# Optimization experiments

Hardware: AMD Instinct MI355X
Metric: run time of the kernel (lower is better)

## Reference

```python
import jax, jax.numpy as jnp
import numpy as np

BATCH = 32      # init batch_size
HID = 256       # init hidden_dim
SENT = 64       # sentence_size
WORDS = 64      # words per sentence (the -1 in the view)
N = BATCH * SENT


def setup_inputs() -> dict:
    key = jax.random.key(0)
    k1, k2, k3, k4 = jax.random.split(key, 4)
    stdv_lin = 1.0 / np.sqrt(HID)
    x = jax.random.normal(k1, (N, WORDS, HID), dtype=jnp.float32)
    W = jax.random.uniform(k2, (HID, HID), jnp.float32, -stdv_lin, stdv_lin)
    b = jax.random.uniform(k3, (HID,), jnp.float32, -stdv_lin, stdv_lin)
    context = jax.random.uniform(k4, (HID,), jnp.float32, -stdv_lin, stdv_lin)
    return {"x": x, "W": W, "b": b, "context": context, "sentence_size": SENT}


def reference(x, W, b, context, sentence_size):
    # tanh(Linear(x)) applied per position; vectorized over the batch loop
    attends = jnp.tanh(jnp.einsum("nwh,oh->nwo", x, W) + b)  # [N, WORDS, HID]
    scores = attends * context                                 # [N, WORDS, HID]
    # nn.Softmax on the [-1, HID] view -> softmax over the hidden dim
    alpha = jax.nn.softmax(scores, axis=-1)                    # [N, WORDS, HID]
    attended = x * alpha                                       # legacy same-numel mul
    attended = attended.reshape(BATCH, sentence_size, -1, HID)
    return jnp.sum(attended, axis=2)                           # [BATCH, SENT, HID]
```

## Files before the change

kernel.cpp:

```cpp
#include <hip/hip_runtime.h>
#include <hip/hip_bf16.h>

#define HID 256
#define NROWS 2048
#define NITER 8
#define GRID (NROWS / NITER)
#define PITCH 264
#define AS1 __attribute__((address_space(1)))
#define AS3 __attribute__((address_space(3)))

typedef __attribute__((ext_vector_type(8))) short short8;
typedef __attribute__((ext_vector_type(4))) float float4v;
typedef __attribute__((ext_vector_type(4))) unsigned short ushort4v;

__device__ __forceinline__ float bf2f(unsigned short u) {
    return __uint_as_float(((unsigned int)u) << 16);
}

__device__ __forceinline__ unsigned int pk_bf16(float a, float b) {
    __hip_bfloat162 p = __float22bfloat162_rn(float2{a, b});
    return *(unsigned int*)&p;
}

__device__ __forceinline__ float tanh_fast(float x) {
    float e = __builtin_amdgcn_exp2f(x * 2.8853900817779268f);
    return 1.0f - 2.0f * __builtin_amdgcn_rcpf(e + 1.0f);
}

__device__ __forceinline__ float exp_small(float s) {
    float p = __builtin_fmaf(s, 0.16666667f, 0.5f);
    p = __builtin_fmaf(p, s, 1.0f);
    return __builtin_fmaf(p, s, 1.0f);
}

__device__ __forceinline__ float row16_sum(float v) {
    float t;
    t = __builtin_bit_cast(float, __builtin_amdgcn_update_dpp(
            0, __builtin_bit_cast(int, v), 0xB1, 0xf, 0xf, true));
    v += t;
    t = __builtin_bit_cast(float, __builtin_amdgcn_update_dpp(
            0, __builtin_bit_cast(int, v), 0x4E, 0xf, 0xf, true));
    v += t;
    t = __builtin_bit_cast(float, __builtin_amdgcn_update_dpp(
            0, __builtin_bit_cast(int, v), 0x124, 0xf, 0xf, true));
    v += t;
    t = __builtin_bit_cast(float, __builtin_amdgcn_update_dpp(
            0, __builtin_bit_cast(int, v), 0x128, 0xf, 0xf, true));
    v += t;
    return v;
}

__global__ void cvt_w(const float* __restrict__ W, unsigned short* __restrict__ Wb) {
    int i = blockIdx.x * 256 + threadIdx.x;
    float4v v = ((const float4v*)W)[i];
    unsigned int lo = pk_bf16(v.x, v.y), hi = pk_bf16(v.z, v.w);
    ushort4v u;
    u.x = (unsigned short)lo; u.y = (unsigned short)(lo >> 16);
    u.z = (unsigned short)hi; u.w = (unsigned short)(hi >> 16);
    ((ushort4v*)Wb)[i] = u;
}

__global__ __launch_bounds__(512, 2) void attend_fused(
    const float* __restrict__ x, const unsigned short* __restrict__ Wb,
    const float* __restrict__ bias, const float* __restrict__ ctx,
    float* __restrict__ out)
{
    __shared__ float fstage[64 * 256];
    __shared__ unsigned short xs[64 * PITCH];
    __shared__ float wsum[8][64];
    __shared__ float rinv[64];

    const int tid  = threadIdx.x;
    const int wave = tid >> 6;
    const int lane = tid & 63;
    const int q    = lane >> 4;
    const int c    = lane & 15;
    const int obase = wave * 32;

    float bb[2], cc[2];
#pragma unroll
    for (int nt = 0; nt < 2; ++nt) {
        bb[nt] = bias[obase + 2 * c + nt];
        cc[nt] = ctx[obase + 2 * c + nt];
    }
    short8 bfrag[8][2];
#pragma unroll
    for (int nt = 0; nt < 2; ++nt) {
        const unsigned short* wr = &Wb[(size_t)(obase + 2 * c + nt) * 256 + q * 8];
#pragma unroll
        for (int kt = 0; kt < 8; ++kt)
            bfrag[kt][nt] = *(const short8*)(wr + kt * 32);
    }

    const int n0 = blockIdx.x * NITER;

    {
        const float* xn = x + (size_t)n0 * (64 * 256);
#pragma unroll
        for (int t = 0; t < 8; ++t) {
            const int row = wave * 8 + t;
            __builtin_amdgcn_global_load_lds((const AS1 void*)(xn + row * 256 + lane * 4),
                                             (AS3 void*)&fstage[row * 256], 16, 0, 0);
        }
    }

    for (int it = 0; it < NITER; ++it) {
        const int n = n0 + it;
        const float* xnext = x + (size_t)(n + 1) * (64 * 256);
        const bool pf = (it + 1 < NITER);

        __syncthreads();

#pragma unroll
        for (int i = 0; i < 8; ++i) {
            const int chunk = tid + 512 * i;
            const int r = chunk >> 6, col4 = (chunk & 63) * 4;
            float4v v = *(const float4v*)&fstage[chunk * 4];
            uint2 u;
            u.x = pk_bf16(v.x, v.y);
            u.y = pk_bf16(v.z, v.w);
            *(uint2*)&xs[r * PITCH + col4] = u;
        }
        __syncthreads();

        if (pf) {
#pragma unroll
            for (int t = 0; t < 4; ++t) {
                const int row = wave * 8 + t;
                __builtin_amdgcn_global_load_lds((const AS1 void*)(xnext + row * 256 + lane * 4),
                                                 (AS3 void*)&fstage[row * 256], 16, 0, 0);
            }
        }

        float4v acc[4][2];
#pragma unroll
        for (int mt = 0; mt < 4; ++mt)
#pragma unroll
            for (int nt = 0; nt < 2; ++nt)
                acc[mt][nt] = (float4v){0.f, 0.f, 0.f, 0.f};

#pragma unroll
        for (int kt = 0; kt < 8; ++kt) {
            short8 a[4];
#pragma unroll
            for (int mt = 0; mt < 4; ++mt)
                a[mt] = *(const short8*)&xs[(mt * 16 + c) * PITCH + kt * 32 + q * 8];
#pragma unroll
            for (int nt = 0; nt < 2; ++nt)
#pragma unroll
                for (int mt = 0; mt < 4; ++mt)
                    acc[mt][nt] = __builtin_amdgcn_mfma_f32_16x16x32_bf16(
                        a[mt], bfrag[kt][nt], acc[mt][nt], 0, 0, 0);
        }

        float psum[4][4];
#pragma unroll
        for (int mt = 0; mt < 4; ++mt)
#pragma unroll
            for (int r = 0; r < 4; ++r)
                psum[mt][r] = 0.f;

#pragma unroll
        for (int nt = 0; nt < 2; ++nt) {
#pragma unroll
            for (int mt = 0; mt < 4; ++mt) {
#pragma unroll
                for (int r = 0; r < 4; ++r) {
                    float s = tanh_fast(acc[mt][nt][r] + bb[nt]) * cc[nt];
                    float e = exp_small(s);
                    acc[mt][nt][r] = e;
                    psum[mt][r] += e;
                }
            }
        }
#pragma unroll
        for (int mt = 0; mt < 4; ++mt)
#pragma unroll
            for (int r = 0; r < 4; ++r)
                psum[mt][r] = row16_sum(psum[mt][r]);
        if (c == 0) {
#pragma unroll
            for (int mt = 0; mt < 4; ++mt)
#pragma unroll
                for (int r = 0; r < 4; ++r)
                    wsum[wave][mt * 16 + q * 4 + r] = psum[mt][r];
        }
        __syncthreads();
        if (tid < 64) {
            float t = wsum[0][tid] + wsum[1][tid] + wsum[2][tid] + wsum[3][tid]
                    + wsum[4][tid] + wsum[5][tid] + wsum[6][tid] + wsum[7][tid];
            rinv[tid] = __builtin_amdgcn_rcpf(t);
        }
        __syncthreads();

        if (pf) {
#pragma unroll
            for (int t = 4; t < 8; ++t) {
                const int row = wave * 8 + t;
                __builtin_amdgcn_global_load_lds((const AS1 void*)(xnext + row * 256 + lane * 4),
                                                 (AS3 void*)&fstage[row * 256], 16, 0, 0);
            }
        }

        float ri[4][4];
#pragma unroll
        for (int mt = 0; mt < 4; ++mt)
#pragma unroll
            for (int r = 0; r < 4; ++r)
                ri[mt][r] = rinv[mt * 16 + q * 4 + r];

        float outp[2] = {0.f, 0.f};
#pragma unroll
        for (int mt = 0; mt < 4; ++mt) {
#pragma unroll
            for (int r = 0; r < 4; ++r) {
                const int w = mt * 16 + q * 4 + r;
                unsigned int pair = *(const unsigned int*)&xs[w * PITCH + obase + 2 * c];
                const float wgt = ri[mt][r];
                outp[0] += bf2f((unsigned short)pair)         * (acc[mt][0][r] * wgt);
                outp[1] += bf2f((unsigned short)(pair >> 16)) * (acc[mt][1][r] * wgt);
            }
        }
#pragma unroll
        for (int nt = 0; nt < 2; ++nt) {
            float v = outp[nt];
            v += __shfl_xor(v, 16);
            v += __shfl_xor(v, 32);
            outp[nt] = v;
        }
        if (q == 0)
            *(float2*)&out[(size_t)n * HID + obase + 2 * c] = float2{outp[0], outp[1]};
    }
}

extern "C" void kernel_launch(void* const* d_in, const int* in_sizes, int n_in,
                              void* d_out, int out_size, void* d_ws, size_t ws_size,
                              hipStream_t stream) {
    const float* x    = (const float*)d_in[0];
    const float* W    = (const float*)d_in[1];
    const float* bias = (const float*)d_in[2];
    const float* ctx  = (const float*)d_in[3];
    unsigned short* Wb = (unsigned short*)d_ws;

    cvt_w<<<64, 256, 0, stream>>>(W, Wb);
    attend_fused<<<GRID, 512, 0, stream>>>(x, Wb, bias, ctx, (float*)d_out);
}
```

Before: 208.4 us.

## Register-prefetch x into double-buffered bf16 LDS tiles and fuse W conversion

Replaces the global_load_lds fp32 staging buffer with register prefetch of the next x tile, which is converted to bf16 straight into a double-buffered LDS tile at the end of each iteration. This removes the fp32 LDS round trip and one barrier per iteration. The separate W-to-bf16 conversion kernel is dropped and W is converted at load time in every block, saving a launch but repeating the conversion in each block. The softmax exponent is computed exactly as exp(c)*exp2(-2c*rd) rather than through a cubic polynomial, adding one exp per element. Holding 8 float4 prefetch registers raises register pressure under launch_bounds(512,2).

```diff
diff --git a/kernel.cpp b/kernel.cpp
--- a/kernel.cpp
+++ b/kernel.cpp
@@ -6,12 +6,11 @@
 #define NITER 8
 #define GRID (NROWS / NITER)
 #define PITCH 264
-#define AS1 __attribute__((address_space(1)))
-#define AS3 __attribute__((address_space(3)))
+#define TILE_F (64 * 256)
 
 typedef __attribute__((ext_vector_type(8))) short short8;
 typedef __attribute__((ext_vector_type(4))) float float4v;
-typedef __attribute__((ext_vector_type(4))) unsigned short ushort4v;
+typedef __attribute__((ext_vector_type(4))) unsigned int uint4v;
 
 __device__ __forceinline__ float bf2f(unsigned short u) {
     return __uint_as_float(((unsigned int)u) << 16);
@@ -22,15 +21,11 @@
     return *(unsigned int*)&p;
 }
 
-__device__ __forceinline__ float tanh_fast(float x) {
-    float e = __builtin_amdgcn_exp2f(x * 2.8853900817779268f);
-    return 1.0f - 2.0f * __builtin_amdgcn_rcpf(e + 1.0f);
-}
-
-__device__ __forceinline__ float exp_small(float s) {
-    float p = __builtin_fmaf(s, 0.16666667f, 0.5f);
-    p = __builtin_fmaf(p, s, 1.0f);
-    return __builtin_fmaf(p, s, 1.0f);
+__device__ __forceinline__ void bar_sync() {
+    __builtin_amdgcn_sched_barrier(0);
+    asm volatile("s_waitcnt lgkmcnt(0)");
+    __builtin_amdgcn_s_barrier();
+    __builtin_amdgcn_sched_barrier(0);
 }
 
 __device__ __forceinline__ float row16_sum(float v) {
@@ -50,23 +45,12 @@
     return v;
 }
 
-__global__ void cvt_w(const float* __restrict__ W, unsigned short* __restrict__ Wb) {
-    int i = blockIdx.x * 256 + threadIdx.x;
-    float4v v = ((const float4v*)W)[i];
-    unsigned int lo = pk_bf16(v.x, v.y), hi = pk_bf16(v.z, v.w);
-    ushort4v u;
-    u.x = (unsigned short)lo; u.y = (unsigned short)(lo >> 16);
-    u.z = (unsigned short)hi; u.w = (unsigned short)(hi >> 16);
-    ((ushort4v*)Wb)[i] = u;
-}
-
 __global__ __launch_bounds__(512, 2) void attend_fused(
-    const float* __restrict__ x, const unsigned short* __restrict__ Wb,
+    const float* __restrict__ x, const float* __restrict__ W,
     const float* __restrict__ bias, const float* __restrict__ ctx,
     float* __restrict__ out)
 {
-    __shared__ float fstage[64 * 256];
-    __shared__ unsigned short xs[64 * PITCH];
+    __shared__ unsigned short xs[2][64 * PITCH];
     __shared__ float wsum[8][64];
     __shared__ float rinv[64];
 
@@ -76,61 +60,55 @@
     const int q    = lane >> 4;
     const int c    = lane & 15;
     const int obase = wave * 32;
-
-    float bb[2], cc[2];
+    const int n0 = blockIdx.x * NITER;
+
+    float4v R[8];
+    {
+        const float4v* xv = (const float4v*)(x + (size_t)n0 * TILE_F);
+#pragma unroll
+        for (int i = 0; i < 8; ++i) R[i] = xv[tid + 512 * i];
+    }
+
+    float bb[2], m2[2], ec[2];
+    short8 bfrag[8][2];
 #pragma unroll
     for (int nt = 0; nt < 2; ++nt) {
-        bb[nt] = bias[obase + 2 * c + nt];
-        cc[nt] = ctx[obase + 2 * c + nt];
-    }
-    short8 bfrag[8][2];
-#pragma unroll
-    for (int nt = 0; nt < 2; ++nt) {
-        const unsigned short* wr = &Wb[(size_t)(obase + 2 * c + nt) * 256 + q * 8];
-#pragma unroll
-        for (int kt = 0; kt < 8; ++kt)
-            bfrag[kt][nt] = *(const short8*)(wr + kt * 32);
-    }
-
-    const int n0 = blockIdx.x * NITER;
-
+        const int o = obase + 2 * c + nt;
+        bb[nt] = bias[o];
+        const float cv = ctx[o];
+        m2[nt] = cv * -2.8853900817779268f;
+        ec[nt] = __builtin_amdgcn_exp2f(cv * 1.4426950408889634f);
+        const float* wr = W + (size_t)o * 256 + q * 8;
+#pragma unroll
+        for (int kt = 0; kt < 8; ++kt) {
+            float4v w0 = *(const float4v*)(wr + kt * 32);
+            float4v w1 = *(const float4v*)(wr + kt * 32 + 4);
+            uint4v u = { pk_bf16(w0.x, w0.y), pk_bf16(w0.z, w0.w),
+                         pk_bf16(w1.x, w1.y), pk_bf16(w1.z, w1.w) };
+            bfrag[kt][nt] = __builtin_bit_cast(short8, u);
+        }
+    }
+
+#pragma unroll
+    for (int i = 0; i < 8; ++i) {
+        const int chunk = tid + 512 * i;
+        const int r = chunk >> 6, col4 = (chunk & 63) * 4;
+        uint2 u;
+        u.x = pk_bf16(R[i].x, R[i].y);
+        u.y = pk_bf16(R[i].z, R[i].w);
+        *(uint2*)&xs[0][r * PITCH + col4] = u;
+    }
     {
-        const float* xn = x + (size_t)n0 * (64 * 256);
-#pragma unroll
-        for (int t = 0; t < 8; ++t) {
-            const int row = wave * 8 + t;
-            __builtin_amdgcn_global_load_lds((const AS1 void*)(xn + row * 256 + lane * 4),
-                                             (AS3 void*)&fstage[row * 256], 16, 0, 0);
-        }
-    }
-
+        const float4v* xv = (const float4v*)(x + (size_t)(n0 + 1) * TILE_F);
+#pragma unroll
+        for (int i = 0; i < 8; ++i) R[i] = xv[tid + 512 * i];
+    }
+    bar_sync();
+
+    int cur = 0;
+#pragma unroll 1
     for (int it = 0; it < NITER; ++it) {
-        const int n = n0 + it;
-        const float* xnext = x + (size_t)(n + 1) * (64 * 256);
-        const bool pf = (it + 1 < NITER);
-
-        __syncthreads();
-
-#pragma unroll
-        for (int i = 0; i < 8; ++i) {
-            const int chunk = tid + 512 * i;
-            const int r = chunk >> 6, col4 = (chunk & 63) * 4;
-            float4v v = *(const float4v*)&fstage[chunk * 4];
-            uint2 u;
-            u.x = pk_bf16(v.x, v.y);
-            u.y = pk_bf16(v.z, v.w);
-            *(uint2*)&xs[r * PITCH + col4] = u;
-        }
-        __syncthreads();
-
-        if (pf) {
-#pragma unroll
-            for (int t = 0; t < 4; ++t) {
-                const int row = wave * 8 + t;
-                __builtin_amdgcn_global_load_lds((const AS1 void*)(xnext + row * 256 + lane * 4),
-                                                 (AS3 void*)&fstage[row * 256], 16, 0, 0);
-            }
-        }
+        const unsigned short* xsc = xs[cur];
 
         float4v acc[4][2];
 #pragma unroll
@@ -144,7 +122,7 @@
             short8 a[4];
 #pragma unroll
             for (int mt = 0; mt < 4; ++mt)
-                a[mt] = *(const short8*)&xs[(mt * 16 + c) * PITCH + kt * 32 + q * 8];
+                a[mt] = *(const short8*)&xsc[(mt * 16 + c) * PITCH + kt * 32 + q * 8];
 #pragma unroll
             for (int nt = 0; nt < 2; ++nt)
 #pragma unroll
@@ -166,8 +144,10 @@
             for (int mt = 0; mt < 4; ++mt) {
 #pragma unroll
                 for (int r = 0; r < 4; ++r) {
-                    float s = tanh_fast(acc[mt][nt][r] + bb[nt]) * cc[nt];
-                    float e = exp_small(s);
+                    const float y  = acc[mt][nt][r] + bb[nt];
+                    const float E  = __builtin_amdgcn_exp2f(y * 2.8853900817779268f);
+                    const float rd = __builtin_amdgcn_rcpf(E + 1.0f);
+                    const float e  = ec[nt] * __builtin_amdgcn_exp2f(m2[nt] * rd);
                     acc[mt][nt][r] = e;
                     psum[mt][r] += e;
                 }
@@ -180,27 +160,18 @@
                 psum[mt][r] = row16_sum(psum[mt][r]);
         if (c == 0) {
 #pragma unroll
-            for (int mt = 0; mt < 4; ++mt)
-#pragma unroll
-                for (int r = 0; r < 4; ++r)
-                    wsum[wave][mt * 16 + q * 4 + r] = psum[mt][r];
-        }
-        __syncthreads();
+            for (int mt = 0; mt < 4; ++mt) {
+                float4v p = {psum[mt][0], psum[mt][1], psum[mt][2], psum[mt][3]};
+                *(float4v*)&wsum[wave][mt * 16 + q * 4] = p;
+            }
+        }
+        bar_sync();
         if (tid < 64) {
-            float t = wsum[0][tid] + wsum[1][tid] + wsum[2][tid] + wsum[3][tid]
-                    + wsum[4][tid] + wsum[5][tid] + wsum[6][tid] + wsum[7][tid];
+            const float t = wsum[0][tid] + wsum[1][tid] + wsum[2][tid] + wsum[3][tid]
+                          + wsum[4][tid] + wsum[5][tid] + wsum[6][tid] + wsum[7][tid];
             rinv[tid] = __builtin_amdgcn_rcpf(t);
         }
-        __syncthreads();
-
-        if (pf) {
-#pragma unroll
-            for (int t = 4; t < 8; ++t) {
-                const int row = wave * 8 + t;
-                __builtin_amdgcn_global_load_lds((const AS1 void*)(xnext + row * 256 + lane * 4),
-                                                 (AS3 void*)&fstage[row * 256], 16, 0, 0);
-            }
-        }
+        bar_sync();
 
         float ri[4][4];
 #pragma unroll
@@ -215,7 +186,7 @@
 #pragma unroll
             for (int r = 0; r < 4; ++r) {
                 const int w = mt * 16 + q * 4 + r;
-                unsigned int pair = *(const unsigned int*)&xs[w * PITCH + obase + 2 * c];
+                unsigned int pair = *(const unsigned int*)&xsc[w * PITCH + obase + 2 * c];
                 const float wgt = ri[mt][r];
                 outp[0] += bf2f((unsigned short)pair)         * (acc[mt][0][r] * wgt);
                 outp[1] += bf2f((unsigned short)(pair >> 16)) * (acc[mt][1][r] * wgt);
@@ -229,7 +200,27 @@
             outp[nt] = v;
         }
         if (q == 0)
-            *(float2*)&out[(size_t)n * HID + obase + 2 * c] = float2{outp[0], outp[1]};
+            *(float2*)&out[(size_t)(n0 + it) * HID + obase + 2 * c] = float2{outp[0], outp[1]};
+
+        if (it + 1 < NITER) {
+            unsigned short* xsn = (unsigned short*)xs[cur ^ 1];
+#pragma unroll
+            for (int i = 0; i < 8; ++i) {
+                const int chunk = tid + 512 * i;
+                const int r = chunk >> 6, col4 = (chunk & 63) * 4;
+                uint2 u;
+                u.x = pk_bf16(R[i].x, R[i].y);
+                u.y = pk_bf16(R[i].z, R[i].w);
+                *(uint2*)&xsn[r * PITCH + col4] = u;
+            }
+            if (it + 2 < NITER) {
+                const float4v* xv = (const float4v*)(x + (size_t)(n0 + it + 2) * TILE_F);
+#pragma unroll
+                for (int i = 0; i < 8; ++i) R[i] = xv[tid + 512 * i];
+            }
+        }
+        bar_sync();
+        cur ^= 1;
     }
 }
 
@@ -240,8 +231,7 @@
     const float* W    = (const float*)d_in[1];
     const float* bias = (const float*)d_in[2];
     const float* ctx  = (const float*)d_in[3];
-    unsigned short* Wb = (unsigned short*)d_ws;
-
-    cvt_w<<<64, 256, 0, stream>>>(W, Wb);
-    attend_fused<<<GRID, 512, 0, stream>>>(x, Wb, bias, ctx, (float*)d_out);
-}
+    (void)in_sizes; (void)n_in; (void)d_ws; (void)ws_size;
+
+    attend_fused<<<GRID, 512, 0, stream>>>(x, W, bias, ctx, (float*)d_out);
+}
```

After: 207.4 us. No clear change (-0.5%).
